# Kernel optimization log

Hardware: AMD Instinct MI355X
Metric: run time of the kernel (lower is better)

## Reference

```python
import jax, jax.numpy as jnp
import numpy as np
from jax import lax

B, L, T = 16, 400, 200
N_MELS, ENC, PRE = 80, 512, 256
QH, DH, ATTN = 1024, 1024, 128
NFILT, K = 32, 31
PAD = (K - 1) // 2  # 15


def setup_inputs() -> dict:
    key = jax.random.key(0)
    ks = jax.random.split(key, 20)
    def w(k, shape, s=0.05):
        return jax.random.normal(k, shape, dtype=jnp.float32) * s
    return {
        "memory": w(ks[0], (B, L, ENC), 1.0),
        "memory_lengths": jnp.full((B,), L, dtype=jnp.int32),
        "teacher": w(ks[1], (B, T, N_MELS), 1.0),
        # prenet (Linear bias=False x2)
        "pre_w1": w(ks[2], (PRE, N_MELS)),
        "pre_w2": w(ks[3], (PRE, PRE)),
        # query_rnn LSTMCell (input = prenet_dim + enc_embed_dim)
        "q_wih": w(ks[4], (4 * QH, PRE + ENC)),
        "q_whh": w(ks[5], (4 * QH, QH)),
        "q_bih": jnp.zeros((4 * QH,), jnp.float32),
        "q_bhh": jnp.zeros((4 * QH,), jnp.float32),
        # dec_rnn LSTMCell (input = query_rnn_dim + enc_embed_dim)
        "d_wih": w(ks[6], (4 * DH, QH + ENC)),
        "d_whh": w(ks[7], (4 * DH, DH)),
        "d_bih": jnp.zeros((4 * DH,), jnp.float32),
        "d_bhh": jnp.zeros((4 * DH,), jnp.float32),
        # location-sensitive attention
        "attn_wq": w(ks[8], (ATTN, QH)),
        "attn_wm": w(ks[9], (ATTN, ENC)),
        "attn_conv": w(ks[10], (NFILT, 2, K)),  # Conv1d(2 -> NFILT, k=31), bias=False
        "attn_wloc": w(ks[11], (ATTN, NFILT)),
        "attn_v": w(ks[12], (1, ATTN)),
        # output projections
        "proj_w": w(ks[13], (N_MELS, DH + ENC)),
        "proj_b": jnp.zeros((N_MELS,), jnp.float32),
        "gate_w": w(ks[14], (1, DH + ENC)),
        "gate_b": jnp.zeros((1,), jnp.float32),
    }


def _prenet(x, w1, w2):
    # dropout p=0 -> identity
    x = jax.nn.relu(x @ w1.T)
    return jax.nn.relu(x @ w2.T)


def _lstm_cell(x, h, c, wih, whh, bih, bhh):
    z = x @ wih.T + h @ whh.T + bih + bhh
    i, f, g, o = jnp.split(z, 4, axis=-1)  # torch LSTMCell gate order
    c = jax.nn.sigmoid(f) * c + jax.nn.sigmoid(i) * jnp.tanh(g)
    h = jax.nn.sigmoid(o) * jnp.tanh(c)
    return h, c


def reference(memory, memory_lengths, teacher, pre_w1, pre_w2,
              q_wih, q_whh, q_bih, q_bhh, d_wih, d_whh, d_bih, d_bhh,
              attn_wq, attn_wm, attn_conv, attn_wloc, attn_v,
              proj_w, proj_b, gate_w, gate_b):
    del memory_lengths  # forward() sets mask = None unconditionally
    processed_memory = memory @ attn_wm.T            # (B, L, ATTN)

    # teacher-forced prenet inputs (tf_rate=1.0, drop_dec_in=0.0)
    go = _prenet(jnp.zeros((B, N_MELS), memory.dtype), pre_w1, pre_w2)  # (B, PRE)
    tpre = _prenet(teacher, pre_w1, pre_w2)          # (B, T, PRE)
    dec_ins = jnp.concatenate([go[:, None], tpre[:, :-1]], axis=1)       # (B, T, PRE)
    dec_ins = dec_ins.transpose(1, 0, 2)             # (T, B, PRE)

    z = lambda *s: jnp.zeros(s, memory.dtype)
    carry0 = (z(B, QH), z(B, QH), z(B, DH), z(B, DH), z(B, L), z(B, L), z(B, ENC))

    def step(carry, dec_in):
        qh, qc, dh, dc, aw, aws, ctx = carry
        qh, qc = _lstm_cell(jnp.concatenate([dec_in, ctx], -1), qh, qc,
                            q_wih, q_whh, q_bih, q_bhh)
        # location-sensitive attention
        hist = jnp.stack([aw, aws], axis=1)          # (B, 2, L)
        loc = lax.conv_general_dilated(hist, attn_conv, (1,), [(PAD, PAD)],
                                       dimension_numbers=("NCH", "OIH", "NCH"))  # (B, NFILT, L)
        loc = jnp.einsum("bfl,af->bla", loc, attn_wloc)          # (B, L, ATTN)
        pq = (qh @ attn_wq.T)[:, None, :]                         # (B, 1, ATTN)
        energies = jnp.tanh(pq + loc + processed_memory) @ attn_v[0]  # (B, L)
        weights = jax.nn.softmax(energies, axis=-1)               # (B, L)
        ctx = jnp.einsum("bl,ble->be", weights, memory)           # (B, ENC)
        aws = aws + weights
        dh, dc = _lstm_cell(jnp.concatenate([ctx, qh], -1), dh, dc,
                            d_wih, d_whh, d_bih, d_bhh)
        feat = jnp.concatenate([dh, ctx], -1)                     # (B, DH+ENC)
        mel = feat @ proj_w.T + proj_b                            # (B, N_MELS)
        stop = jax.nn.sigmoid(feat @ gate_w.T + gate_b)[:, 0]     # (B,)
        return (qh, qc, dh, dc, weights, aws, ctx), (mel, weights, stop)

    _, (mels, aligns, stops) = lax.scan(step, carry0, dec_ins)
    mel_outputs = mels.transpose(1, 0, 2)      # (B, T, n_mels)  (n_frames_per_step=1)
    alignments = aligns.transpose(1, 0, 2)     # (B, T, L)
    stops = stops.transpose(1, 0)              # (B, T)
    return mel_outputs, alignments, stops
```

## Files before the change

kernel.cpp:

```cpp
#include <hip/hip_runtime.h>
#include <math.h>

#define Bsz 16
#define Lsz 400
#define Tsz 200
#define NMELS 80
#define ENC 512
#define PREsz 256
#define QHsz 1024
#define DHsz 1024
#define ATTNsz 128
#define NFILT 32
#define KW 31
#define PADW 15

typedef const float* __restrict__ cfp;
typedef float* __restrict__ fp;
typedef __fp16 hf;
typedef __fp16 h2 __attribute__((ext_vector_type(2)));
typedef const hf* __restrict__ chp;

union F4H { float4 f; h2 h[4]; };

__device__ __forceinline__ float4 ldf4(const float* p){ return *reinterpret_cast<const float4*>(p); }
__device__ __forceinline__ float sigm(float x){ return 1.0f/(1.0f + __expf(-x)); }
__device__ __forceinline__ float tanhfast(float x){
  x = fminf(fmaxf(x, -15.0f), 15.0f);
  float e = __expf(2.0f*x);
  return (e-1.0f)/(e+1.0f);
}
__device__ __forceinline__ h2 pk2(float a, float b){
  return __builtin_amdgcn_cvt_pkrtz(a, b);
}
__device__ __forceinline__ float fdot2f(h2 a, h2 b, float c){
#if __has_builtin(__builtin_amdgcn_fdot2)
  return __builtin_amdgcn_fdot2(a, b, c, false);
#else
  return c + (float)a.x*(float)b.x + (float)a.y*(float)b.y;
#endif
}

__global__ void kzero(fp p, int n){
  int i = blockIdx.x*256 + threadIdx.x;
  if (i < n) p[i] = 0.0f;
}

__global__ void kcvt(cfp src, hf* __restrict__ dst, int n){
  int i = (blockIdx.x*256 + threadIdx.x)*4;
  if (i + 3 < n){
    float4 v = ldf4(src + i);
    dst[i+0] = (hf)v.x; dst[i+1] = (hf)v.y; dst[i+2] = (hf)v.z; dst[i+3] = (hf)v.w;
  } else {
    for (int k=i; k<n; k++) dst[k] = (hf)src[k];
  }
}

__global__ void __launch_bounds__(256) kprenet2(cfp teacher, cfp w1, cfp w2, fp dec_ins){
  int b = blockIdx.x & 15, tc = blockIdx.x >> 4;
  int t0 = tc*16;
  int tid = threadIdx.x;
  __shared__ __align__(16) float tch[16][80];
  __shared__ __align__(16) float h1[16][256];
  for (int idx = tid; idx < 16*80; idx += 256){
    int i = idx / 80, k = idx % 80;
    int t = t0 + i;
    float v = 0.f;
    if (t >= 1 && t < Tsz) v = teacher[((size_t)b*Tsz + (t-1))*NMELS + k];
    tch[i][k] = v;
  }
  __syncthreads();
  {
    int r = tid;
    float acc[16];
    #pragma unroll
    for (int i=0;i<16;i++) acc[i]=0.f;
    const float* wr = w1 + (size_t)r*80;
    for (int k=0;k<80;k++){
      float w = wr[k];
      #pragma unroll
      for (int i=0;i<16;i++) acc[i] += w * tch[i][k];
    }
    #pragma unroll
    for (int i=0;i<16;i++) h1[i][r] = fmaxf(acc[i], 0.f);
  }
  __syncthreads();
  {
    int r = tid;
    float acc[16];
    #pragma unroll
    for (int i=0;i<16;i++) acc[i]=0.f;
    const float* wr = w2 + (size_t)r*256;
    for (int k=0;k<256;k++){
      float w = wr[k];
      #pragma unroll
      for (int i=0;i<16;i++) acc[i] += w * h1[i][k];
    }
    for (int i=0;i<16;i++){
      int t = t0 + i;
      if (t < Tsz){
        float v = (t == 0) ? 0.f : fmaxf(acc[i], 0.f);
        dec_ins[((size_t)t*Bsz + b)*PREsz + r] = v;
      }
    }
  }
}

__global__ void __launch_bounds__(256) kpm2(cfp memory, cfp wm, fp pm){
  int b = blockIdx.x / 25, lc = blockIdx.x % 25;
  int l0 = lc*16;
  int tid = threadIdx.x;
  __shared__ __align__(16) float mrow[16][512];
  {
    const float4* s4 = (const float4*)(memory + ((size_t)b*Lsz + l0)*ENC);
    float4* d4 = (float4*)&mrow[0][0];
    #pragma unroll
    for (int i=0;i<8;i++) d4[tid + i*256] = s4[tid + i*256];
  }
  __syncthreads();
  int a = tid & 127, g = tid >> 7;
  const float* wr = wm + (size_t)a*ENC;
  float acc[8];
  #pragma unroll
  for (int i=0;i<8;i++) acc[i]=0.f;
  for (int k=0;k<512;k+=4){
    float4 w4 = ldf4(wr + k);
    #pragma unroll
    for (int i=0;i<8;i++){
      float4 x4 = ldf4(&mrow[g*8+i][k]);
      acc[i] += w4.x*x4.x + w4.y*x4.y + w4.z*x4.z + w4.w*x4.w;
    }
  }
  #pragma unroll
  for (int i=0;i<8;i++)
    pm[((size_t)b*Lsz + l0 + g*8 + i)*ATTNsz + a] = acc[i];
}

struct GateSmem { __align__(16) h2 xsh[16][132]; };
struct ConvSmem { float hists[2][80]; float convo[NFILT][50]; float cwsh[NFILT*2*KW]; float stat2[2]; };
union SMemA { GateSmem g; ConvSmem c; };

__global__ void __launch_bounds__(256) kgatesA(
    int t, int do_q, int do_d,
    cfp dec_ins, cfp qh_state, cfp dh_state,
    cfp cpartP, cfp emaxP, cfp esumP, cfp ebufP,
    cfp awsP, fp awsQ,
    fp qpart, fp dpart, fp loc, fp out_align,
    chp h_qwih, chp h_qwhh, chp h_dwih, chp h_dwhh,
    cfp conv_w, cfp wloc)
{
  int bid = blockIdx.x, tid = threadIdx.x;
  __shared__ SMemA sm;

  if (bid >= 144){
    int gid = bid - 144;
    int isq = (gid < 896);
    if (isq ? !do_q : !do_d) return;
    int idx = isq ? gid : (gid - 896);
    int nch = isq ? 7 : 10;
    int c = idx % nch, rg = idx / nch;
    int bb = tid >> 4, quar = tid & 15;
    int is_ctx = isq ? (c >= 1 && c <= 2) : (c <= 1);
    int ctxoff = isq ? (c-1)*256 : c*256;
    h2* dst = &sm.g.xsh[bb][quar*8];
    if (is_ctx){
      if (!do_d){
        h2 z = pk2(0.f, 0.f);
        #pragma unroll
        for (int i=0;i<8;i++) dst[i] = z;
      } else {
        float m0=emaxP[bb*4+0], m1=emaxP[bb*4+1], m2=emaxP[bb*4+2], m3=emaxP[bb*4+3];
        float gm = fmaxf(fmaxf(m0,m1), fmaxf(m2,m3));
        float e0=__expf(m0-gm), e1=__expf(m1-gm), e2=__expf(m2-gm), e3=__expf(m3-gm);
        float gs = esumP[bb*4+0]*e0 + esumP[bb*4+1]*e1 + esumP[bb*4+2]*e2 + esumP[bb*4+3]*e3;
        float inv = 1.0f/gs;
        float s0=e0*inv, s1=e1*inv, s2=e2*inv, s3=e3*inv;
        const float* cp = cpartP + (size_t)bb*2048 + ctxoff + quar*16;
        #pragma unroll
        for (int kk=0;kk<16;kk+=4){
          float4 p0 = ldf4(cp+kk), p1 = ldf4(cp+512+kk), p2 = ldf4(cp+1024+kk), p3 = ldf4(cp+1536+kk);
          float ax = s0*p0.x + s1*p1.x + s2*p2.x + s3*p3.x;
          float ay = s0*p0.y + s1*p1.y + s2*p2.y + s3*p3.y;
          float az = s0*p0.z + s1*p1.z + s2*p2.z + s3*p3.z;
          float aw = s0*p0.w + s1*p1.w + s2*p2.w + s3*p3.w;
          dst[(kk>>1)+0] = pk2(ax, ay);
          dst[(kk>>1)+1] = pk2(az, aw);
        }
      }
    } else {
      const float* src;
      if (isq){
        if (c == 0)      src = dec_ins + (size_t)t*Bsz*PREsz + bb*PREsz;
        else             src = qh_state + bb*QHsz + (c-3)*256;
      } else {
        if (c < 6)       src = qh_state + bb*QHsz + (c-2)*256;
        else             src = dh_state + bb*DHsz + (c-6)*256;
      }
      const float4* s4 = (const float4*)(src + quar*16);
      float4 t0=s4[0], t1=s4[1], t2=s4[2], t3=s4[3];
      dst[0]=pk2(t0.x,t0.y); dst[1]=pk2(t0.z,t0.w);
      dst[2]=pk2(t1.x,t1.y); dst[3]=pk2(t1.z,t1.w);
      dst[4]=pk2(t2.x,t2.y); dst[5]=pk2(t2.z,t2.w);
      dst[6]=pk2(t3.x,t3.y); dst[7]=pk2(t3.z,t3.w);
    }
    __syncthreads();
    int b = tid & 15, rl = tid >> 4;
    int row0 = rg*32 + rl*2;
    const hf* wbase; int wstride, woff;
    if (isq){
      if (c < 3){ wbase = h_qwih; wstride = 768;  woff = c*256; }
      else      { wbase = h_qwhh; wstride = 1024; woff = (c-3)*256; }
    } else {
      if (c < 6){ wbase = h_dwih; wstride = 1536; woff = c*256; }
      else      { wbase = h_dwhh; wstride = 1024; woff = (c-6)*256; }
    }
    const h2* w0 = (const h2*)(wbase + (size_t)row0*wstride + woff);
    const h2* w1 = (const h2*)(wbase + (size_t)(row0+1)*wstride + woff);
    const h2* xr = &sm.g.xsh[b][0];
    float a0=0.f, a1=0.f;
    #pragma unroll 4
    for (int kb=0; kb<128; kb+=8){
      F4H u0, u1, u2, u3, xA, xB;
      u0.f = ldf4((const float*)(w0 + kb));
      u1.f = ldf4((const float*)(w0 + kb + 4));
      u2.f = ldf4((const float*)(w1 + kb));
      u3.f = ldf4((const float*)(w1 + kb + 4));
      xA.f = ldf4((const float*)(xr + kb));
      xB.f = ldf4((const float*)(xr + kb + 4));
      #pragma unroll
      for (int j=0;j<4;j++){
        a0 = fdot2f(u0.h[j], xA.h[j], a0);
        a0 = fdot2f(u1.h[j], xB.h[j], a0);
        a1 = fdot2f(u2.h[j], xA.h[j], a1);
        a1 = fdot2f(u3.h[j], xB.h[j], a1);
      }
    }
    float2 out = {a0, a1};
    fp part = isq ? qpart : dpart;
    *reinterpret_cast<float2*>(part + ((size_t)(c*16 + b))*4096 + row0) = out;
  } else if (bid < 128){
    if (!do_q) return;
    int cb = bid;
    int b = cb >> 3, chunk = cb & 7;
    int l0 = chunk*50;
    for (int i=tid; i<NFILT*2*KW; i+=256) sm.c.cwsh[i] = conv_w[i];
    if (tid == 0 && do_d){
      float m0=emaxP[b*4+0], m1=emaxP[b*4+1], m2=emaxP[b*4+2], m3=emaxP[b*4+3];
      float gm = fmaxf(fmaxf(m0,m1), fmaxf(m2,m3));
      float gs = esumP[b*4+0]*__expf(m0-gm) + esumP[b*4+1]*__expf(m1-gm)
               + esumP[b*4+2]*__expf(m2-gm) + esumP[b*4+3]*__expf(m3-gm);
      sm.c.stat2[0] = gm; sm.c.stat2[1] = 1.0f/gs;
    }
    __syncthreads();
    float gm = sm.c.stat2[0], ginv = sm.c.stat2[1];
    for (int i=tid; i<80; i+=256){
      int pos = l0 - PADW + i;
      float w = 0.f, as = 0.f;
      if (do_d && pos >= 0 && pos < Lsz){
        w = __expf(ebufP[b*Lsz + pos] - gm) * ginv;
        as = awsP[b*Lsz + pos] + w;
      }
      sm.c.hists[0][i] = w;
      sm.c.hists[1][i] = as;
    }
    __syncthreads();
    for (int task=tid; task<NFILT*50; task+=256){
      int f = task & 31, ll = task >> 5;
      float a = 0.0f;
      const float* c0 = &sm.c.cwsh[(f*2+0)*KW];
      const float* c1 = &sm.c.cwsh[(f*2+1)*KW];
      #pragma unroll
      for (int k=0;k<KW;k++) a += sm.c.hists[0][ll+k]*c0[k] + sm.c.hists[1][ll+k]*c1[k];
      sm.c.convo[f][ll] = a;
    }
    __syncthreads();
    for (int task=tid; task<50*ATTNsz; task+=256){
      int a = task & 127, ll = task >> 7;
      float s = 0.0f;
      const float* wl = wloc + a*NFILT;
      #pragma unroll
      for (int f=0;f<NFILT;f++) s += sm.c.convo[f][ll]*wl[f];
      loc[((size_t)b*Lsz + l0 + ll)*ATTNsz + a] = s;
    }
  } else {
    if (!do_d) return;
    int b = bid - 128;
    __shared__ float st2[2];
    if (tid == 0){
      float m0=emaxP[b*4+0], m1=emaxP[b*4+1], m2=emaxP[b*4+2], m3=emaxP[b*4+3];
      float gm = fmaxf(fmaxf(m0,m1), fmaxf(m2,m3));
      float gs = esumP[b*4+0]*__expf(m0-gm) + esumP[b*4+1]*__expf(m1-gm)
               + esumP[b*4+2]*__expf(m2-gm) + esumP[b*4+3]*__expf(m3-gm);
      st2[0] = gm; st2[1] = 1.0f/gs;
    }
    __syncthreads();
    float gm = st2[0], ginv = st2[1];
    for (int l=tid; l<Lsz; l+=256){
      float w = __expf(ebufP[b*Lsz + l] - gm) * ginv;
      awsQ[b*Lsz + l] = awsP[b*Lsz + l] + w;
      out_align[((size_t)b*Tsz + (t-1))*Lsz + l] = w;
    }
  }
}

__global__ void __launch_bounds__(256) kmidB(
    int t, int do_q, int do_d,
    cfp qpart, cfp dpart,
    cfp qcP, fp qcQ, fp qh_state,
    cfp dcP, fp dcQ, fp dh_state,
    chp h_wq, cfp vvec, cfp loc, cfp pm, cfp memory,
    cfp cpartP, cfp emaxP, cfp esumP,
    fp cpartQ, fp emaxQ, fp esumQ, fp ebufQ,
    cfp q_bih, cfp q_bhh, cfp d_bih, cfp d_bhh,
    chp h_proj, cfp proj_b, chp h_gate, cfp gate_b,
    fp out_mel, fp out_stop)
{
  int bid = blockIdx.x, tid = threadIdx.x;
  if (bid < 64){
    if (!do_q) return;
    int b = bid & 15, lc = bid >> 4;
    int l0 = lc*100;
    int lane = tid & 63, wv = tid >> 6;
    __shared__ __align__(16) h2 qh2l[512];
    __shared__ float pqv[128], vsh[128];
    __shared__ float esh[100], pesh[100];
    __shared__ float red4[4], red4b[4];
    __shared__ __align__(16) float4 psum[128];
    {
      int j4 = tid*4;
      float4 acc[4];
      #pragma unroll
      for (int g=0; g<4; g++){
        int r4 = g*1024 + j4;
        float4 bi = ldf4(q_bih + r4), bh = ldf4(q_bhh + r4);
        float4 a = {bi.x+bh.x, bi.y+bh.y, bi.z+bh.z, bi.w+bh.w};
        #pragma unroll
        for (int c=0;c<7;c++){
          float4 p = ldf4(qpart + ((size_t)(c*16 + b))*4096 + r4);
          a.x += p.x; a.y += p.y; a.z += p.z; a.w += p.w;
        }
        acc[g] = a;
      }
      float4 zi = acc[0], zf = acc[1], zg = acc[2], zo = acc[3];
      float4 cp = ldf4(qcP + b*QHsz + j4);
      float4 cn, hn;
      cn.x = sigm(zf.x)*cp.x + sigm(zi.x)*tanhfast(zg.x); hn.x = sigm(zo.x)*tanhfast(cn.x);
      cn.y = sigm(zf.y)*cp.y + sigm(zi.y)*tanhfast(zg.y); hn.y = sigm(zo.y)*tanhfast(cn.y);
      cn.z = sigm(zf.z)*cp.z + sigm(zi.z)*tanhfast(zg.z); hn.z = sigm(zo.z)*tanhfast(cn.z);
      cn.w = sigm(zf.w)*cp.w + sigm(zi.w)*tanhfast(zg.w); hn.w = sigm(zo.w)*tanhfast(cn.w);
      if (lc == 0){
        *reinterpret_cast<float4*>(qcQ + b*QHsz + j4) = cn;
        *reinterpret_cast<float4*>(qh_state + b*QHsz + j4) = hn;
      }
      qh2l[tid*2+0] = pk2(hn.x, hn.y);
      qh2l[tid*2+1] = pk2(hn.z, hn.w);
    }
    if (tid < 128) vsh[tid] = vvec[tid];
    __syncthreads();
    {
      int r = tid >> 1, kh = tid & 1;
      const h2* wr = (const h2*)(h_wq + (size_t)r*QHsz + kh*512);
      const h2* xr = &qh2l[kh*256];
      float acc = 0.f;
      #pragma unroll 4
      for (int k=0;k<256;k+=8){
        F4H wA, wB, xA, xB;
        wA.f = ldf4((const float*)(wr + k));
        wB.f = ldf4((const float*)(wr + k + 4));
        xA.f = ldf4((const float*)(xr + k));
        xB.f = ldf4((const float*)(xr + k + 4));
        #pragma unroll
        for (int j=0;j<4;j++){
          acc = fdot2f(wA.h[j], xA.h[j], acc);
          acc = fdot2f(wB.h[j], xB.h[j], acc);
        }
      }
      acc += __shfl_xor(acc, 1, 64);
      if (kh == 0) pqv[r] = acc;
    }
    __syncthreads();
    {
      int ll = tid >> 1, ah = tid & 1;
      float e = 0.f;
      if (ll < 100){
        int l = l0 + ll;
        const float* lp = loc + ((size_t)b*Lsz + l)*ATTNsz + ah*64;
        const float* pp = pm  + ((size_t)b*Lsz + l)*ATTNsz + ah*64;
        const float* pqa = &pqv[ah*64];
        const float* va  = &vsh[ah*64];
        #pragma unroll 4
        for (int a=0;a<64;a+=4){
          float4 l4 = ldf4(lp+a), p4 = ldf4(pp+a);
          e += tanhfast(pqa[a+0]+l4.x+p4.x)*va[a+0];
          e += tanhfast(pqa[a+1]+l4.y+p4.y)*va[a+1];
          e += tanhfast(pqa[a+2]+l4.z+p4.z)*va[a+2];
          e += tanhfast(pqa[a+3]+l4.w+p4.w)*va[a+3];
        }
      }
      e += __shfl_xor(e, 1, 64);
      if (ll < 100 && ah == 0) esh[ll] = e;
    }
    __syncthreads();
    {
      float lm = (tid < 100) ? esh[tid] : -1e30f;
      #pragma unroll
      for (int off=32; off>0; off>>=1) lm = fmaxf(lm, __shfl_xor(lm, off, 64));
      if (lane == 0) red4[wv] = lm;
      __syncthreads();
      float mx = fmaxf(fmaxf(red4[0], red4[1]), fmaxf(red4[2], red4[3]));
      float p = 0.f;
      if (tid < 100){
        p = __expf(esh[tid]-mx);
        pesh[tid] = p;
        ebufQ[b*Lsz + l0 + tid] = esh[tid];
      }
      float ls = p;
      #pragma unroll
      for (int off=32; off>0; off>>=1) ls += __shfl_xor(ls, off, 64);
      if (lane == 0) red4b[wv] = ls;
      __syncthreads();
      if (tid == 0){
        emaxQ[b*4+lc] = mx;
        esumQ[b*4+lc] = red4b[0]+red4b[1]+red4b[2]+red4b[3];
      }
    }
    {
      int e4 = tid & 127, lh = tid >> 7;
      const float* mp = memory + ((size_t)b*Lsz + l0)*ENC + e4*4;
      float4 a = {0.f,0.f,0.f,0.f};
      for (int l = lh*50; l < lh*50+50; l++){
        float w = pesh[l];
        float4 m4 = ldf4(mp + (size_t)l*ENC);
        a.x += w*m4.x; a.y += w*m4.y; a.z += w*m4.z; a.w += w*m4.w;
      }
      if (lh == 1) psum[e4] = a;
      __syncthreads();
      if (lh == 0){
        float4 p = psum[e4];
        a.x += p.x; a.y += p.y; a.z += p.z; a.w += p.w;
        *reinterpret_cast<float4*>(cpartQ + ((size_t)b*4 + lc)*512 + e4*4) = a;
      }
    }
  } else {
    if (!do_d) return;
    int db = bid - 64;
    int b = db & 15, half = db >> 4;
    int tm = t - 1;
    int lane = tid & 63, wv = tid >> 6;
    __shared__ __align__(16) h2 feath[768];
    __shared__ float scs[4];
    {
      int j4 = tid*4;
      float4 acc[4];
      #pragma unroll
      for (int g=0; g<4; g++){
        int r4 = g*1024 + j4;
        float4 bi = ldf4(d_bih + r4), bh = ldf4(d_bhh + r4);
        float4 a = {bi.x+bh.x, bi.y+bh.y, bi.z+bh.z, bi.w+bh.w};
        #pragma unroll
        for (int c=0;c<10;c++){
          float4 p = ldf4(dpart + ((size_t)(c*16 + b))*4096 + r4);
          a.x += p.x; a.y += p.y; a.z += p.z; a.w += p.w;
        }
        acc[g] = a;
      }
      if (tid == 0){
        float m0=emaxP[b*4+0], m1=emaxP[b*4+1], m2=emaxP[b*4+2], m3=emaxP[b*4+3];
        float gm = fmaxf(fmaxf(m0,m1), fmaxf(m2,m3));
        float e0=__expf(m0-gm), e1=__expf(m1-gm), e2=__expf(m2-gm), e3=__expf(m3-gm);
        float gs = esumP[b*4+0]*e0 + esumP[b*4+1]*e1 + esumP[b*4+2]*e2 + esumP[b*4+3]*e3;
        float inv = 1.0f/gs;
        scs[0]=e0*inv; scs[1]=e1*inv; scs[2]=e2*inv; scs[3]=e3*inv;
      }
      float4 zi = acc[0], zf = acc[1], zg = acc[2], zo = acc[3];
      float4 cp = ldf4(dcP + b*DHsz + j4);
      float4 cn, hn;
      cn.x = sigm(zf.x)*cp.x + sigm(zi.x)*tanhfast(zg.x); hn.x = sigm(zo.x)*tanhfast(cn.x);
      cn.y = sigm(zf.y)*cp.y + sigm(zi.y)*tanhfast(zg.y); hn.y = sigm(zo.y)*tanhfast(cn.y);
      cn.z = sigm(zf.z)*cp.z + sigm(zi.z)*tanhfast(zg.z); hn.z = sigm(zo.z)*tanhfast(cn.z);
      cn.w = sigm(zf.w)*cp.w + sigm(zi.w)*tanhfast(zg.w); hn.w = sigm(zo.w)*tanhfast(cn.w);
      if (half == 0){
        *reinterpret_cast<float4*>(dcQ + b*DHsz + j4) = cn;
        *reinterpret_cast<float4*>(dh_state + b*DHsz + j4) = hn;
      }
      feath[tid*2+0] = pk2(hn.x, hn.y);
      feath[tid*2+1] = pk2(hn.z, hn.w);
    }
    __syncthreads();
    {
      float s0=scs[0], s1=scs[1], s2=scs[2], s3=scs[3];
      int i0 = tid*2;
      const float* cp = cpartP + (size_t)b*2048;
      float v0 = s0*cp[i0]   + s1*cp[512+i0]   + s2*cp[1024+i0]   + s3*cp[1536+i0];
      float v1 = s0*cp[i0+1] + s1*cp[512+i0+1] + s2*cp[1024+i0+1] + s3*cp[1536+i0+1];
      feath[512 + tid] = pk2(v0, v1);
    }
    __syncthreads();
    int rbeg = half*40, rend = half ? 81 : 40;
    for (int r = rbeg + wv; r < rend; r += 4){
      const h2* wr = (r < 80) ? (const h2*)(h_proj + (size_t)r*1536) : (const h2*)h_gate;
      float acc = 0.0f;
      #pragma unroll
      for (int m=0;m<3;m++){
        int k4 = (lane + 64*m)*4;
        F4H w, x;
        w.f = ldf4((const float*)(wr + k4));
        x.f = ldf4((const float*)(&feath[k4]));
        #pragma unroll
        for (int j=0;j<4;j++) acc = fdot2f(w.h[j], x.h[j], acc);
      }
      #pragma unroll
      for (int off=32; off>0; off>>=1) acc += __shfl_xor(acc, off, 64);
      if (lane == 0){
        if (r < 80) out_mel[((size_t)b*Tsz + tm)*NMELS + r] = acc + proj_b[r];
        else        out_stop[b*Tsz + tm] = sigm(acc + gate_b[0]);
      }
    }
  }
}

extern "C" void kernel_launch(void* const* d_in, const int* in_sizes, int n_in,
                              void* d_out, int out_size, void* d_ws, size_t ws_size,
                              hipStream_t stream)
{
  const float* memory  = (const float*)d_in[0];
  const float* teacher = (const float*)d_in[2];
  const float* pre_w1  = (const float*)d_in[3];
  const float* pre_w2  = (const float*)d_in[4];
  const float* q_wih   = (const float*)d_in[5];
  const float* q_whh   = (const float*)d_in[6];
  const float* q_bih   = (const float*)d_in[7];
  const float* q_bhh   = (const float*)d_in[8];
  const float* d_wih   = (const float*)d_in[9];
  const float* d_whh   = (const float*)d_in[10];
  const float* d_bih   = (const float*)d_in[11];
  const float* d_bhh   = (const float*)d_in[12];
  const float* attn_wq   = (const float*)d_in[13];
  const float* attn_wm   = (const float*)d_in[14];
  const float* attn_conv = (const float*)d_in[15];
  const float* attn_wloc = (const float*)d_in[16];
  const float* attn_v    = (const float*)d_in[17];
  const float* proj_w  = (const float*)d_in[18];
  const float* proj_b  = (const float*)d_in[19];
  const float* gate_w  = (const float*)d_in[20];
  const float* gate_b  = (const float*)d_in[21];

  float* ws = (float*)d_ws;
  float* dec_ins  = ws;
  float* pm       = dec_ins + 819200;
  float* loc      = pm + 819200;
  float* qpart    = loc + 819200;
  float* dpart    = qpart + 458752;
  float* ebuf2    = dpart + 655360;
  float* emax2    = ebuf2 + 12800;
  float* esum2    = emax2 + 128;
  float* cpart2   = esum2 + 128;
  float* qh_state = cpart2 + 65536;
  float* dh_state = qh_state + 16384;
  float* qc2      = dh_state + 16384;
  float* dc2      = qc2 + 32768;
  float* aws2     = dc2 + 32768;
  float* fend     = aws2 + 12800;

  hf* h_qwih = (hf*)fend;
  hf* h_qwhh = h_qwih + 3145728;
  hf* h_dwih = h_qwhh + 4194304;
  hf* h_dwhh = h_dwih + 6291456;
  hf* h_wq   = h_dwhh + 4194304;
  hf* h_proj = h_wq + 131072;
  hf* h_gate = h_proj + 122880;

  float* out_mel   = (float*)d_out;
  float* out_align = out_mel + (size_t)Bsz*Tsz*NMELS;
  float* out_stop  = out_align + (size_t)Bsz*Tsz*Lsz;

  const int stateN = 16384+16384+32768+32768+12800;
  kzero<<<dim3((stateN+255)/256), dim3(256), 0, stream>>>(qh_state, stateN);
  kcvt<<<dim3(3145728/1024), dim3(256), 0, stream>>>(q_wih, h_qwih, 3145728);
  kcvt<<<dim3(4194304/1024), dim3(256), 0, stream>>>(q_whh, h_qwhh, 4194304);
  kcvt<<<dim3(6291456/1024), dim3(256), 0, stream>>>(d_wih, h_dwih, 6291456);
  kcvt<<<dim3(4194304/1024), dim3(256), 0, stream>>>(d_whh, h_dwhh, 4194304);
  kcvt<<<dim3(131072/1024), dim3(256), 0, stream>>>(attn_wq, h_wq, 131072);
  kcvt<<<dim3(122880/1024), dim3(256), 0, stream>>>(proj_w, h_proj, 122880);
  kcvt<<<dim3(2), dim3(256), 0, stream>>>(gate_w, h_gate, 1536);
  kprenet2<<<dim3(16*13), dim3(256), 0, stream>>>(teacher, pre_w1, pre_w2, dec_ins);
  kpm2<<<dim3(400), dim3(256), 0, stream>>>(memory, attn_wm, pm);

  for (int t = 0; t <= Tsz; t++){
    int pp = (t+1)&1, qq = t&1;
    int do_q = (t < Tsz) ? 1 : 0;
    int do_d = (t > 0) ? 1 : 0;
    kgatesA<<<dim3(2320), dim3(256), 0, stream>>>(
      t, do_q, do_d,
      dec_ins, qh_state, dh_state,
      cpart2 + pp*32768, emax2 + pp*64, esum2 + pp*64, ebuf2 + pp*6400,
      aws2 + pp*6400, aws2 + qq*6400,
      qpart, dpart, loc, out_align,
      h_qwih, h_qwhh, h_dwih, h_dwhh,
      attn_conv, attn_wloc);
    kmidB<<<dim3(96), dim3(256), 0, stream>>>(
      t, do_q, do_d,
      qpart, dpart,
      qc2 + pp*16384, qc2 + qq*16384, qh_state,
      dc2 + pp*16384, dc2 + qq*16384, dh_state,
      h_wq, attn_v, loc, pm, memory,
      cpart2 + pp*32768, emax2 + pp*64, esum2 + pp*64,
      cpart2 + qq*32768, emax2 + qq*64, esum2 + qq*64, ebuf2 + qq*6400,
      q_bih, q_bhh, d_bih, d_bhh,
      h_proj, proj_b, h_gate, gate_b,
      out_mel, out_stop);
  }
}
```

Baseline: 9.710 ms.

## Compute four gate rows per thread and re-layout attention query weights

Each thread in the LSTM gate-GEMV blocks now computes four output rows instead of two. This halves the block count (2320 to 1232) and reuses each shared-memory x load across twice as many rows. The attention query weight matrix is converted into an interleaved half-precision layout so the per-step pq GEMV in kmidB reads weights coalesced across threads instead of with row strides. The trade-offs are fewer blocks in flight to hide the weight streaming and the loop being forced to unroll 1.

```diff
diff --git a/kernel.cpp b/kernel.cpp
--- a/kernel.cpp
+++ b/kernel.cpp
@@ -55,6 +55,17 @@
   }
 }
 
+__global__ void kcvt_wq(cfp src, hf* __restrict__ dst){
+  int idx = blockIdx.x*256 + threadIdx.x;
+  int c = idx >> 8, rk = idx & 255;
+  int r = rk >> 1, kh = rk & 1;
+  const float* s = src + ((size_t)r*1024 + kh*512 + c*8);
+  hf* d = dst + ((size_t)idx)*8;
+  float4 v0 = ldf4(s), v1 = ldf4(s+4);
+  d[0]=(hf)v0.x; d[1]=(hf)v0.y; d[2]=(hf)v0.z; d[3]=(hf)v0.w;
+  d[4]=(hf)v1.x; d[5]=(hf)v1.y; d[6]=(hf)v1.z; d[7]=(hf)v1.w;
+}
+
 __global__ void __launch_bounds__(256) kprenet2(cfp teacher, cfp w1, cfp w2, fp dec_ins){
   int b = blockIdx.x & 15, tc = blockIdx.x >> 4;
   int t0 = tc*16;
@@ -153,9 +164,9 @@
 
   if (bid >= 144){
     int gid = bid - 144;
-    int isq = (gid < 896);
+    int isq = (gid < 448);
     if (isq ? !do_q : !do_d) return;
-    int idx = isq ? gid : (gid - 896);
+    int idx = isq ? gid : (gid - 448);
     int nch = isq ? 7 : 10;
     int c = idx % nch, rg = idx / nch;
     int bb = tid >> 4, quar = tid & 15;
@@ -204,7 +215,7 @@
     }
     __syncthreads();
     int b = tid & 15, rl = tid >> 4;
-    int row0 = rg*32 + rl*2;
+    int row0 = rg*64 + rl*4;
     const hf* wbase; int wstride, woff;
     if (isq){
       if (c < 3){ wbase = h_qwih; wstride = 768;  woff = c*256; }
@@ -213,19 +224,22 @@
       if (c < 6){ wbase = h_dwih; wstride = 1536; woff = c*256; }
       else      { wbase = h_dwhh; wstride = 1024; woff = (c-6)*256; }
     }
-    const h2* w0 = (const h2*)(wbase + (size_t)row0*wstride + woff);
+    const h2* w0 = (const h2*)(wbase + (size_t)(row0+0)*wstride + woff);
     const h2* w1 = (const h2*)(wbase + (size_t)(row0+1)*wstride + woff);
+    const h2* w2 = (const h2*)(wbase + (size_t)(row0+2)*wstride + woff);
+    const h2* w3 = (const h2*)(wbase + (size_t)(row0+3)*wstride + woff);
     const h2* xr = &sm.g.xsh[b][0];
-    float a0=0.f, a1=0.f;
-    #pragma unroll 4
+    float a0=0.f, a1=0.f, a2=0.f, a3=0.f;
+    #pragma unroll 1
     for (int kb=0; kb<128; kb+=8){
-      F4H u0, u1, u2, u3, xA, xB;
+      F4H xA, xB;
+      xA.f = ldf4((const float*)(xr + kb));
+      xB.f = ldf4((const float*)(xr + kb + 4));
+      F4H u0, u1, u2, u3;
       u0.f = ldf4((const float*)(w0 + kb));
       u1.f = ldf4((const float*)(w0 + kb + 4));
       u2.f = ldf4((const float*)(w1 + kb));
       u3.f = ldf4((const float*)(w1 + kb + 4));
-      xA.f = ldf4((const float*)(xr + kb));
-      xB.f = ldf4((const float*)(xr + kb + 4));
       #pragma unroll
       for (int j=0;j<4;j++){
         a0 = fdot2f(u0.h[j], xA.h[j], a0);
@@ -233,10 +247,21 @@
         a1 = fdot2f(u2.h[j], xA.h[j], a1);
         a1 = fdot2f(u3.h[j], xB.h[j], a1);
       }
-    }
-    float2 out = {a0, a1};
+      u0.f = ldf4((const float*)(w2 + kb));
+      u1.f = ldf4((const float*)(w2 + kb + 4));
+      u2.f = ldf4((const float*)(w3 + kb));
+      u3.f = ldf4((const float*)(w3 + kb + 4));
+      #pragma unroll
+      for (int j=0;j<4;j++){
+        a2 = fdot2f(u0.h[j], xA.h[j], a2);
+        a2 = fdot2f(u1.h[j], xB.h[j], a2);
+        a3 = fdot2f(u2.h[j], xA.h[j], a3);
+        a3 = fdot2f(u3.h[j], xB.h[j], a3);
+      }
+    }
+    float4 out = {a0, a1, a2, a3};
     fp part = isq ? qpart : dpart;
-    *reinterpret_cast<float2*>(part + ((size_t)(c*16 + b))*4096 + row0) = out;
+    *reinterpret_cast<float4*>(part + ((size_t)(c*16 + b))*4096 + row0) = out;
   } else if (bid < 128){
     if (!do_q) return;
     int cb = bid;
@@ -357,17 +382,18 @@
     if (tid < 128) vsh[tid] = vvec[tid];
     __syncthreads();
     {
-      int r = tid >> 1, kh = tid & 1;
-      const h2* wr = (const h2*)(h_wq + (size_t)r*QHsz + kh*512);
+      int kh = tid & 1;
+      const h2* wq2 = (const h2*)h_wq;
       const h2* xr = &qh2l[kh*256];
+      int l4 = tid*4;
       float acc = 0.f;
       #pragma unroll 4
-      for (int k=0;k<256;k+=8){
+      for (int c=0;c<64;c+=2){
         F4H wA, wB, xA, xB;
-        wA.f = ldf4((const float*)(wr + k));
-        wB.f = ldf4((const float*)(wr + k + 4));
-        xA.f = ldf4((const float*)(xr + k));
-        xB.f = ldf4((const float*)(xr + k + 4));
+        wA.f = ldf4((const float*)(wq2 + c*1024 + l4));
+        wB.f = ldf4((const float*)(wq2 + (c+1)*1024 + l4));
+        xA.f = ldf4((const float*)(xr + c*4));
+        xB.f = ldf4((const float*)(xr + c*4 + 4));
         #pragma unroll
         for (int j=0;j<4;j++){
           acc = fdot2f(wA.h[j], xA.h[j], acc);
@@ -375,7 +401,7 @@
         }
       }
       acc += __shfl_xor(acc, 1, 64);
-      if (kh == 0) pqv[r] = acc;
+      if (kh == 0) pqv[tid >> 1] = acc;
     }
     __syncthreads();
     {
@@ -579,7 +605,7 @@
   kcvt<<<dim3(4194304/1024), dim3(256), 0, stream>>>(q_whh, h_qwhh, 4194304);
   kcvt<<<dim3(6291456/1024), dim3(256), 0, stream>>>(d_wih, h_dwih, 6291456);
   kcvt<<<dim3(4194304/1024), dim3(256), 0, stream>>>(d_whh, h_dwhh, 4194304);
-  kcvt<<<dim3(131072/1024), dim3(256), 0, stream>>>(attn_wq, h_wq, 131072);
+  kcvt_wq<<<dim3(64), dim3(256), 0, stream>>>(attn_wq, h_wq);
   kcvt<<<dim3(122880/1024), dim3(256), 0, stream>>>(proj_w, h_proj, 122880);
   kcvt<<<dim3(2), dim3(256), 0, stream>>>(gate_w, h_gate, 1536);
   kprenet2<<<dim3(16*13), dim3(256), 0, stream>>>(teacher, pre_w1, pre_w2, dec_ins);
@@ -589,7 +615,7 @@
     int pp = (t+1)&1, qq = t&1;
     int do_q = (t < Tsz) ? 1 : 0;
     int do_d = (t > 0) ? 1 : 0;
-    kgatesA<<<dim3(2320), dim3(256), 0, stream>>>(
+    kgatesA<<<dim3(1232), dim3(256), 0, stream>>>(
       t, do_q, do_d,
       dec_ins, qh_state, dh_state,
       cpart2 + pp*32768, emax2 + pp*64, esum2 + pp*64, ebuf2 + pp*6400,
```

After: 8.839 ms. -9.0%, faster.
